# Performance work log

Measured on AMD Instinct MI355X. Metric: run time of the kernel, lower is better.

Reference implementation:

```python
import jax, jax.numpy as jnp
import numpy as np

EMBED = 128   # embed_dim
HEADS = 8
POINTS = 4
H_SP, W_SP = 51, 102   # hardcoded spatial_shapes in __init__
BEV = 100              # bev_res
HRES = 50              # height_res


def _make_ref_points():
    """Exact numpy replica of the spherical grid built in __init__."""
    eps = 1e-6
    x = np.linspace(-71 / 2, 71 / 2, BEV)
    y = np.linspace(-71 / 2, 71 / 2, BEV)
    z = np.linspace(-50 / 2, 50 / 2, HRES)
    gx, gy, gz = np.meshgrid(x, y, z, indexing='ij')
    phi = np.sign(gy + eps) * np.arccos(gx / (np.sqrt(gx ** 2 + gy ** 2) + eps))
    theta = np.arccos(gz / (np.sqrt(gx ** 2 + gy ** 2 + gz ** 2) + eps))
    phi = 2 * np.pi - phi
    phi[phi > 2 * np.pi] -= 2 * np.pi
    col = phi / (2 * np.pi)   # grd_col_cross
    row = theta / np.pi       # grd_row_cross
    ref = np.stack([col, row], axis=-1)              # (BEV, BEV, HRES, 2)
    ref = ref.transpose(2, 0, 1, 3).reshape(HRES, BEV * BEV, 2)
    return jnp.asarray(ref, dtype=jnp.float32)


def setup_inputs() -> dict:
    key = jax.random.key(0)
    ks = jax.random.split(key, 12)
    d = EMBED
    s = 0.02
    return {
        'query': jax.random.normal(ks[0], (1, BEV * BEV, d), jnp.float32),
        'value': jax.random.normal(ks[1], (1, H_SP * W_SP, d), jnp.float32),
        'ref_points': _make_ref_points(),
        'W_off': jax.random.normal(ks[2], (d, HEADS * POINTS * 2), jnp.float32) * s,
        'b_off': jax.random.normal(ks[3], (HEADS * POINTS * 2,), jnp.float32) * s,
        'W_attn': jax.random.normal(ks[4], (d, HEADS * POINTS), jnp.float32) * s,
        'b_attn': jax.random.normal(ks[5], (HEADS * POINTS,), jnp.float32) * s,
        'W_val': jax.random.normal(ks[6], (d, d), jnp.float32) * s,
        'b_val': jax.random.normal(ks[7], (d,), jnp.float32) * s,
        'W_out': jax.random.normal(ks[8], (d, d), jnp.float32) * s,
        'b_out': jax.random.normal(ks[9], (d,), jnp.float32) * s,
        'W_proj': jax.random.normal(ks[10], (d, 1), jnp.float32) * s,
        'b_proj': jax.random.normal(ks[11], (1,), jnp.float32) * s,
    }


def _bilinear_sample(vflat, loc):
    """grid_sample(bilinear, zero padding, align_corners=False).
    vflat: (B, H*W, hd) value maps; loc: (B, N, 2) normalized [0,1] (x,y)."""
    px = loc[..., 0] * W_SP - 0.5
    py = loc[..., 1] * H_SP - 0.5
    x0 = jnp.floor(px)
    y0 = jnp.floor(py)
    dx = (px - x0)[..., None]
    dy = (py - y0)[..., None]
    x0i = x0.astype(jnp.int32)
    y0i = y0.astype(jnp.int32)

    def gather(xi, yi):
        valid = (xi >= 0) & (xi < W_SP) & (yi >= 0) & (yi < H_SP)
        idx = jnp.clip(yi, 0, H_SP - 1) * W_SP + jnp.clip(xi, 0, W_SP - 1)
        v = jnp.take_along_axis(vflat, idx[..., None], axis=1)  # (B, N, hd)
        return v * valid[..., None].astype(vflat.dtype)

    v00 = gather(x0i, y0i)
    v01 = gather(x0i + 1, y0i)
    v10 = gather(x0i, y0i + 1)
    v11 = gather(x0i + 1, y0i + 1)
    return (v00 * (1 - dx) * (1 - dy) + v01 * dx * (1 - dy)
            + v10 * (1 - dx) * dy + v11 * dx * dy)


def reference(query, value, ref_points, W_off, b_off, W_attn, b_attn,
              W_val, b_val, W_out, b_out, W_proj, b_proj):
    bs, nq, d = query.shape
    hd = d // HEADS
    L = ref_points.shape[0]

    # query-dependent MSDA projections (identical across height levels)
    offsets = (query @ W_off + b_off).reshape(bs, nq, HEADS, POINTS, 2)
    aw = jax.nn.softmax((query @ W_attn + b_attn).reshape(bs, nq, HEADS, POINTS), axis=-1)
    awt = aw.transpose(0, 2, 1, 3)                              # (bs, heads, nq, points)
    v = (value @ W_val + b_val).reshape(bs, -1, HEADS, hd)
    vflat = v.transpose(0, 2, 1, 3).reshape(bs * HEADS, H_SP * W_SP, hd)
    norm = jnp.asarray([W_SP, H_SP], dtype=query.dtype)         # offset_normalizer [W, H]

    def per_level(ref):  # ref: (nq, 2) -> MSDA output with its internal residual
        loc = ref[None, :, None, None, :] + offsets / norm      # (bs, nq, heads, pts, 2)
        loc = loc.transpose(0, 2, 1, 3, 4).reshape(bs * HEADS, nq * POINTS, 2)
        samp = _bilinear_sample(vflat, loc).reshape(bs, HEADS, nq, POINTS, hd)
        out = jnp.einsum('bhnp,bhnpd->bnhd', awt, samp).reshape(bs, nq, d)
        return out @ W_out + b_out + query                      # mmcv MSDA adds identity

    grd = jax.vmap(per_level)(ref_points)                       # (L, bs, nq, d)
    grd_3d = grd.transpose(1, 2, 0, 3).reshape(bs, BEV, BEV, L, d)
    weights = jax.nn.softmax(grd_3d @ W_proj + b_proj, axis=3)  # (bs, BEV, BEV, L, 1)
    max_height_index = jnp.argmax(weights, axis=3)              # (bs, BEV, BEV, 1)
    grd_bev = (weights * grd_3d).sum(axis=3)                    # (bs, BEV, BEV, d)
    return grd_bev.reshape(bs, nq, d) + query, max_height_index
```

## Files before the change

### kernel.cpp

```cpp
#include <hip/hip_runtime.h>
#include <math.h>

#define EMBED   128
#define NHEADS  8
#define NPOINTS 4
#define HD      16
#define HSP     51
#define WSP     102
#define NPIX    (HSP * WSP)
#define NQ      10000
#define NLVL    50

#define GRID_A ((NPIX + 7) / 8)
#define GRID_B (NQ / 8)

__global__ __launch_bounds__(256) void k_prep(
    const float* __restrict__ value,
    const float* __restrict__ Wv,
    const float* __restrict__ bv,
    const float* __restrict__ query,
    const float* __restrict__ Woff,
    const float* __restrict__ boff,
    const float* __restrict__ Wattn,
    const float* __restrict__ battn,
    const float* __restrict__ Wout,
    const float* __restrict__ Wproj,
    float* __restrict__ vout,
    float* __restrict__ off_out,
    float* __restrict__ aw_out,
    float* __restrict__ u_out) {
    const int b = blockIdx.x;
    const int t = threadIdx.x;
    __shared__ float srow[8][EMBED];

    if (b < GRID_A) {
        const int p   = t >> 5;
        const int s   = t & 31;
        const int pix = b * 8 + p;
        const int pl  = min(pix, NPIX - 1);
        *(float4*)&srow[p][s * 4] =
            *(const float4*)(value + (size_t)pl * EMBED + s * 4);
        __syncthreads();
        float4 acc = *(const float4*)(bv + s * 4);
        const float* vr = srow[p];
        const float* wp = Wv + s * 4;
#pragma unroll 8
        for (int k = 0; k < EMBED; ++k) {
            const float qv = vr[k];
            const float4 w4 = *(const float4*)(wp + (size_t)k * EMBED);
            acc.x = fmaf(qv, w4.x, acc.x);
            acc.y = fmaf(qv, w4.y, acc.y);
            acc.z = fmaf(qv, w4.z, acc.z);
            acc.w = fmaf(qv, w4.w, acc.w);
        }
        if (pix < NPIX) {
            *(float4*)(vout + (size_t)pix * EMBED + s * 4) = acc;
        }
    } else if (b < GRID_A + GRID_B) {
        const int qi = t >> 5;
        const int s  = t & 31;
        const int q  = (b - GRID_A) * 8 + qi;
        *(float4*)&srow[qi][s * 4] =
            *(const float4*)(query + (size_t)q * EMBED + s * 4);
        __syncthreads();
        if (s < 24) {
            const float* vr = srow[qi];
            const float* wp;
            int wstride;
            float4 acc;
            if (s < 16) {
                wp = Woff + s * 4; wstride = 64;
                acc = *(const float4*)(boff + s * 4);
            } else {
                wp = Wattn + (s - 16) * 4; wstride = 32;
                acc = *(const float4*)(battn + (s - 16) * 4);
            }
#pragma unroll 8
            for (int k = 0; k < EMBED; ++k) {
                const float qv = vr[k];
                const float4 w4 = *(const float4*)(wp + (size_t)k * wstride);
                acc.x = fmaf(qv, w4.x, acc.x);
                acc.y = fmaf(qv, w4.y, acc.y);
                acc.z = fmaf(qv, w4.z, acc.z);
                acc.w = fmaf(qv, w4.w, acc.w);
            }
            if (s < 16) {
                *(float4*)(off_out + (size_t)q * 64 + s * 4) = acc;
            } else {
                const float mx = fmaxf(fmaxf(acc.x, acc.y), fmaxf(acc.z, acc.w));
                const float e0 = __expf(acc.x - mx), e1 = __expf(acc.y - mx);
                const float e2 = __expf(acc.z - mx), e3 = __expf(acc.w - mx);
                const float inv = 1.f / (e0 + e1 + e2 + e3);
                float4 r;
                r.x = e0 * inv; r.y = e1 * inv; r.z = e2 * inv; r.w = e3 * inv;
                *(float4*)(aw_out + (size_t)q * 32 + (s - 16) * 4) = r;
            }
        }
    } else {
        if (t < EMBED) {
            float acc = 0.f;
#pragma unroll 8
            for (int d = 0; d < EMBED; ++d)
                acc = fmaf(Wout[(size_t)t * EMBED + d], Wproj[d], acc);
            u_out[t] = acc;
        }
    }
}

__global__ __launch_bounds__(256, 4) void k_main(
    const float* __restrict__ query,
    const float* __restrict__ refp,
    const float* __restrict__ voff,
    const float* __restrict__ vaw,
    const float* __restrict__ vflat,
    const float* __restrict__ uvec,
    const float* __restrict__ Wout,
    const float* __restrict__ bout,
    float* __restrict__ out0,
    float* __restrict__ out1) {
    const int t = threadIdx.x;
    const int qslot = t >> 7;
    const int w2 = (t >> 6) & 1;
    const int half = (t >> 5) & 1;
    const int sub = t & 31;
    const int h  = sub >> 2;
    const int c4 = sub & 3;
    const int q = blockIdx.x * 2 + qslot;

    __shared__ float  s_rpy[2][NLVL];
    __shared__ float4 s_acc[2][32];
    __shared__ float  s_z[2], s_m[2];
    __shared__ int    s_b[2];

    if (t < 2 * NLVL) {
        const int ql = t / NLVL, l = t - ql * NLVL;
        const int qq = blockIdx.x * 2 + ql;
        s_rpy[ql][l] = refp[((size_t)l * NQ + qq) * 2 + 1];
    }

    const float4* offp = (const float4*)(voff + (size_t)q * 64 + h * 8);
    const float4 o01 = offp[0];
    const float4 o23 = offp[1];
    const float4 awv4 = *(const float4*)(vaw + (size_t)q * 32 + h * 4);
    const float4 u4 = *(const float4*)(uvec + h * 16 + c4 * 4);
    const float rpx = refp[(size_t)q * 2];
    const float4* vbase = (const float4*)vflat + h * 4 + c4;

    const float offx[4] = {o01.x, o01.z, o23.x, o23.z};
    const float offy[4] = {o01.y, o01.w, o23.y, o23.w};
    const float awv[4]  = {awv4.x, awv4.y, awv4.z, awv4.w};

    float wx0[NPOINTS], wx1[NPOINTS], oyc[NPOINTS];
    int xo0[NPOINTS], xo1[NPOINTS];
#pragma unroll
    for (int p = 0; p < NPOINTS; ++p) {
        const float px = fmaf(rpx, (float)WSP, offx[p]) - 0.5f;
        const float fx = floorf(px);
        const float dx = px - fx;
        const int x0 = (int)fx, x1 = x0 + 1;
        const float a = awv[p];
        wx0[p] = ((unsigned)x0 < (unsigned)WSP) ? a * (1.f - dx) : 0.f;
        wx1[p] = ((unsigned)x1 < (unsigned)WSP) ? a * dx : 0.f;
        xo0[p] = min(max(x0, 0), WSP - 1) * 32;
        xo1[p] = min(max(x1, 0), WSP - 1) * 32;
        oyc[p] = offy[p] - 0.5f;
    }

    __syncthreads();

    float4 acc = {0.f, 0.f, 0.f, 0.f};
    float Z = 0.f, m = -1e30f;
    int best = 0;

#pragma unroll 1
    for (int i = 0; i < 13; ++i) {
        if (4 * i + (w2 << 1) >= NLVL) break;
        const int l = 4 * i + (w2 << 1) + half;
        const float rpy = s_rpy[qslot][l];

        float4 v00[NPOINTS], v01[NPOINTS], v10[NPOINTS], v11[NPOINTS];
        float w00[NPOINTS], w01[NPOINTS], w10[NPOINTS], w11[NPOINTS];
#pragma unroll
        for (int p = 0; p < NPOINTS; ++p) {
            const float py = fmaf(rpy, (float)HSP, oyc[p]);
            const float fy = floorf(py);
            const float dy = py - fy;
            const int y0 = (int)fy, y1 = y0 + 1;
            const float t0 = ((unsigned)y0 < (unsigned)HSP) ? (1.f - dy) : 0.f;
            const float t1 = ((unsigned)y1 < (unsigned)HSP) ? dy : 0.f;
            const int rb0 = min(max(y0, 0), HSP - 1) * (WSP * 32);
            const int rb1 = min(max(y1, 0), HSP - 1) * (WSP * 32);
            v00[p] = vbase[rb0 + xo0[p]];
            v01[p] = vbase[rb0 + xo1[p]];
            v10[p] = vbase[rb1 + xo0[p]];
            v11[p] = vbase[rb1 + xo1[p]];
            w00[p] = wx0[p] * t0;
            w01[p] = wx1[p] * t0;
            w10[p] = wx0[p] * t1;
            w11[p] = wx1[p] * t1;
        }
        float4 s = {0.f, 0.f, 0.f, 0.f};
#pragma unroll
        for (int p = 0; p < NPOINTS; ++p) {
            s.x = fmaf(w00[p], v00[p].x, s.x); s.y = fmaf(w00[p], v00[p].y, s.y);
            s.z = fmaf(w00[p], v00[p].z, s.z); s.w = fmaf(w00[p], v00[p].w, s.w);
            s.x = fmaf(w01[p], v01[p].x, s.x); s.y = fmaf(w01[p], v01[p].y, s.y);
            s.z = fmaf(w01[p], v01[p].z, s.z); s.w = fmaf(w01[p], v01[p].w, s.w);
            s.x = fmaf(w10[p], v10[p].x, s.x); s.y = fmaf(w10[p], v10[p].y, s.y);
            s.z = fmaf(w10[p], v10[p].z, s.z); s.w = fmaf(w10[p], v10[p].w, s.w);
            s.x = fmaf(w11[p], v11[p].x, s.x); s.y = fmaf(w11[p], v11[p].y, s.y);
            s.z = fmaf(w11[p], v11[p].z, s.z); s.w = fmaf(w11[p], v11[p].w, s.w);
        }
        float part = s.x * u4.x;
        part = fmaf(s.y, u4.y, part);
        part = fmaf(s.z, u4.z, part);
        part = fmaf(s.w, u4.w, part);
#pragma unroll
        for (int d = 1; d < 32; d <<= 1)
            part += __shfl_xor(part, d, 64);
        const float e = __expf(part);
        Z += e;
        acc.x = fmaf(e, s.x, acc.x);
        acc.y = fmaf(e, s.y, acc.y);
        acc.z = fmaf(e, s.z, acc.z);
        acc.w = fmaf(e, s.w, acc.w);
        best = (part > m) ? l : best;
        m = fmaxf(part, m);
    }

    {
        const float mo = __shfl_xor(m, 32, 64);
        const int   bo = __shfl_xor(best, 32, 64);
        const float Zo = __shfl_xor(Z, 32, 64);
        const float ax = __shfl_xor(acc.x, 32, 64);
        const float ay = __shfl_xor(acc.y, 32, 64);
        const float az = __shfl_xor(acc.z, 32, 64);
        const float aw_ = __shfl_xor(acc.w, 32, 64);
        const bool takeOther = (mo > m) || (mo == m && bo < best);
        best = takeOther ? bo : best;
        m = fmaxf(m, mo);
        Z += Zo;
        acc.x += ax; acc.y += ay; acc.z += az; acc.w += aw_;
    }

    if (w2 == 1) {
        if (half == 0) s_acc[qslot][sub] = acc;
        if ((t & 63) == 0) { s_z[qslot] = Z; s_m[qslot] = m; s_b[qslot] = best; }
    }
    __syncthreads();

    if (w2 == 0) {
        const float4 ao = s_acc[qslot][sub];
        const float Zo = s_z[qslot];
        const float mo = s_m[qslot];
        const int   bo = s_b[qslot];
        const bool takeOther = (mo > m) || (mo == m && bo < best);
        best = takeOther ? bo : best;
        Z += Zo;
        acc.x += ao.x; acc.y += ao.y; acc.z += ao.z; acc.w += ao.w;

        const float inv = 1.f / Z;
        if (half == 0) {
            float4 sv;
            sv.x = acc.x * inv; sv.y = acc.y * inv;
            sv.z = acc.z * inv; sv.w = acc.w * inv;
            s_acc[qslot][sub] = sv;
            if (sub == 0) out1[q] = (float)best;
        }

        const int dpb = sub * 4;
        float4 r = {0.f, 0.f, 0.f, 0.f};
        if (half == 0) {
            const float4 b4 = *(const float4*)(bout + dpb);
            const float4 q4 = *(const float4*)(query + (size_t)q * EMBED + dpb);
            r.x = fmaf(2.f, q4.x, b4.x);
            r.y = fmaf(2.f, q4.y, b4.y);
            r.z = fmaf(2.f, q4.z, b4.z);
            r.w = fmaf(2.f, q4.w, b4.w);
        }
        const float4* srow = s_acc[qslot];
        const int cg0 = half * 16;
#pragma unroll 4
        for (int cg = cg0; cg < cg0 + 16; ++cg) {
            const float4 s4 = srow[cg];
            const float4 w0 = *(const float4*)(Wout + (size_t)(cg * 4 + 0) * EMBED + dpb);
            const float4 w1 = *(const float4*)(Wout + (size_t)(cg * 4 + 1) * EMBED + dpb);
            const float4 w2v = *(const float4*)(Wout + (size_t)(cg * 4 + 2) * EMBED + dpb);
            const float4 w3 = *(const float4*)(Wout + (size_t)(cg * 4 + 3) * EMBED + dpb);
            r.x = fmaf(s4.x, w0.x, r.x); r.y = fmaf(s4.x, w0.y, r.y);
            r.z = fmaf(s4.x, w0.z, r.z); r.w = fmaf(s4.x, w0.w, r.w);
            r.x = fmaf(s4.y, w1.x, r.x); r.y = fmaf(s4.y, w1.y, r.y);
            r.z = fmaf(s4.y, w1.z, r.z); r.w = fmaf(s4.y, w1.w, r.w);
            r.x = fmaf(s4.z, w2v.x, r.x); r.y = fmaf(s4.z, w2v.y, r.y);
            r.z = fmaf(s4.z, w2v.z, r.z); r.w = fmaf(s4.z, w2v.w, r.w);
            r.x = fmaf(s4.w, w3.x, r.x); r.y = fmaf(s4.w, w3.y, r.y);
            r.z = fmaf(s4.w, w3.z, r.z); r.w = fmaf(s4.w, w3.w, r.w);
        }
        {
            const float rx = __shfl_xor(r.x, 32, 64);
            const float ry = __shfl_xor(r.y, 32, 64);
            const float rz = __shfl_xor(r.z, 32, 64);
            const float rw = __shfl_xor(r.w, 32, 64);
            r.x += rx; r.y += ry; r.z += rz; r.w += rw;
        }
        if (half == 0)
            *(float4*)(out0 + (size_t)q * EMBED + dpb) = r;
    }
}

extern "C" void kernel_launch(void* const* d_in, const int* in_sizes, int n_in,
                              void* d_out, int out_size, void* d_ws, size_t ws_size,
                              hipStream_t stream) {
    const float* query = (const float*)d_in[0];
    const float* value = (const float*)d_in[1];
    const float* refp  = (const float*)d_in[2];
    const float* Woff  = (const float*)d_in[3];
    const float* boff  = (const float*)d_in[4];
    const float* Wattn = (const float*)d_in[5];
    const float* battn = (const float*)d_in[6];
    const float* Wval  = (const float*)d_in[7];
    const float* bval  = (const float*)d_in[8];
    const float* Wout  = (const float*)d_in[9];
    const float* bout  = (const float*)d_in[10];
    const float* Wproj = (const float*)d_in[11];

    float* ws = (float*)d_ws;
    float* ws_v   = ws;
    float* ws_off = ws_v + (size_t)NPIX * EMBED;
    float* ws_aw  = ws_off + (size_t)NQ * 64;
    float* ws_u   = ws_aw + (size_t)NQ * 32;

    float* out0 = (float*)d_out;
    float* out1 = out0 + (size_t)NQ * EMBED;

    hipLaunchKernelGGL(k_prep, dim3(GRID_A + GRID_B + 1), dim3(256), 0, stream,
                       value, Wval, bval, query, Woff, boff, Wattn, battn,
                       Wout, Wproj, ws_v, ws_off, ws_aw, ws_u);
    hipLaunchKernelGGL(k_main, dim3(NQ / 2), dim3(256), 0, stream,
                       query, refp, ws_off, ws_aw, ws_v, ws_u, Wout, bout,
                       out0, out1);
}
```

Measured before the change: 250.5 us.

## Precompute per-head projection score map to decouple softmax from value sampling

Precomputes, in the prep kernel, a per-pixel per-head scalar map g = v·u (value projected onto Wout·Wproj), so the height-softmax logits can be obtained by bilinearly sampling this scalar map instead of reducing the full sampled vectors. The main kernel now runs a cheap first pass computing the logits, max and argmax from the scalar map, stores the exp weights in shared memory, then runs the full vector sampling pass using those weights. This removes the dot-product and shuffle reduction from the heavy loop, and launch bounds are raised to allow more resident blocks. Every prep block now recomputes u redundantly, and the extra gather pass adds memory traffic.

```diff
diff --git a/kernel.cpp b/kernel.cpp
--- a/kernel.cpp
+++ b/kernel.cpp
@@ -26,12 +26,13 @@
     const float* __restrict__ Wout,
     const float* __restrict__ Wproj,
     float* __restrict__ vout,
+    float* __restrict__ gout,
     float* __restrict__ off_out,
-    float* __restrict__ aw_out,
-    float* __restrict__ u_out) {
+    float* __restrict__ aw_out) {
     const int b = blockIdx.x;
     const int t = threadIdx.x;
     __shared__ float srow[8][EMBED];
+    __shared__ float4 u_s[32];
 
     if (b < GRID_A) {
         const int p   = t >> 5;
@@ -40,6 +41,30 @@
         const int pl  = min(pix, NPIX - 1);
         *(float4*)&srow[p][s * 4] =
             *(const float4*)(value + (size_t)pl * EMBED + s * 4);
+        if (t < 32) {
+            float4 u4 = {0.f, 0.f, 0.f, 0.f};
+            const float* w0 = Wout + (size_t)(t * 4 + 0) * EMBED;
+            const float* w1 = Wout + (size_t)(t * 4 + 1) * EMBED;
+            const float* w2 = Wout + (size_t)(t * 4 + 2) * EMBED;
+            const float* w3 = Wout + (size_t)(t * 4 + 3) * EMBED;
+#pragma unroll 4
+            for (int d = 0; d < EMBED; d += 4) {
+                const float4 wp = *(const float4*)(Wproj + d);
+                const float4 a = *(const float4*)(w0 + d);
+                const float4 c = *(const float4*)(w1 + d);
+                const float4 e = *(const float4*)(w2 + d);
+                const float4 f = *(const float4*)(w3 + d);
+                u4.x = fmaf(a.x, wp.x, u4.x); u4.x = fmaf(a.y, wp.y, u4.x);
+                u4.x = fmaf(a.z, wp.z, u4.x); u4.x = fmaf(a.w, wp.w, u4.x);
+                u4.y = fmaf(c.x, wp.x, u4.y); u4.y = fmaf(c.y, wp.y, u4.y);
+                u4.y = fmaf(c.z, wp.z, u4.y); u4.y = fmaf(c.w, wp.w, u4.y);
+                u4.z = fmaf(e.x, wp.x, u4.z); u4.z = fmaf(e.y, wp.y, u4.z);
+                u4.z = fmaf(e.z, wp.z, u4.z); u4.z = fmaf(e.w, wp.w, u4.z);
+                u4.w = fmaf(f.x, wp.x, u4.w); u4.w = fmaf(f.y, wp.y, u4.w);
+                u4.w = fmaf(f.z, wp.z, u4.w); u4.w = fmaf(f.w, wp.w, u4.w);
+            }
+            u_s[t] = u4;
+        }
         __syncthreads();
         float4 acc = *(const float4*)(bv + s * 4);
         const float* vr = srow[p];
@@ -53,8 +78,17 @@
             acc.z = fmaf(qv, w4.z, acc.z);
             acc.w = fmaf(qv, w4.w, acc.w);
         }
+        const float4 u4 = u_s[s];
+        float gp = acc.x * u4.x;
+        gp = fmaf(acc.y, u4.y, gp);
+        gp = fmaf(acc.z, u4.z, gp);
+        gp = fmaf(acc.w, u4.w, gp);
+        gp += __shfl_xor(gp, 1, 64);
+        gp += __shfl_xor(gp, 2, 64);
         if (pix < NPIX) {
             *(float4*)(vout + (size_t)pix * EMBED + s * 4) = acc;
+            if ((s & 3) == 0)
+                gout[(size_t)pix * NHEADS + (s >> 2)] = gp;
         }
     } else if (b < GRID_A + GRID_B) {
         const int qi = t >> 5;
@@ -96,24 +130,16 @@
                 *(float4*)(aw_out + (size_t)q * 32 + (s - 16) * 4) = r;
             }
         }
-    } else {
-        if (t < EMBED) {
-            float acc = 0.f;
-#pragma unroll 8
-            for (int d = 0; d < EMBED; ++d)
-                acc = fmaf(Wout[(size_t)t * EMBED + d], Wproj[d], acc);
-            u_out[t] = acc;
-        }
     }
 }
 
-__global__ __launch_bounds__(256, 4) void k_main(
+__global__ __launch_bounds__(256, 6) void k_main(
     const float* __restrict__ query,
     const float* __restrict__ refp,
     const float* __restrict__ voff,
     const float* __restrict__ vaw,
     const float* __restrict__ vflat,
-    const float* __restrict__ uvec,
+    const float* __restrict__ gmap,
     const float* __restrict__ Wout,
     const float* __restrict__ bout,
     float* __restrict__ out0,
@@ -131,6 +157,7 @@
     __shared__ float4 s_acc[2][32];
     __shared__ float  s_z[2], s_m[2];
     __shared__ int    s_b[2];
+    __shared__ float  s_e[2][2][2][13];
 
     if (t < 2 * NLVL) {
         const int ql = t / NLVL, l = t - ql * NLVL;
@@ -142,7 +169,6 @@
     const float4 o01 = offp[0];
     const float4 o23 = offp[1];
     const float4 awv4 = *(const float4*)(vaw + (size_t)q * 32 + h * 4);
-    const float4 u4 = *(const float4*)(uvec + h * 16 + c4 * 4);
     const float rpx = refp[(size_t)q * 2];
     const float4* vbase = (const float4*)vflat + h * 4 + c4;
 
@@ -166,15 +192,59 @@
         oyc[p] = offy[p] - 0.5f;
     }
 
+    const float offx_c = (c4 == 0) ? o01.x : (c4 == 1) ? o01.z : (c4 == 2) ? o23.x : o23.z;
+    const float offy_c = (c4 == 0) ? o01.y : (c4 == 1) ? o01.w : (c4 == 2) ? o23.y : o23.w;
+    const float a_c    = (c4 == 0) ? awv4.x : (c4 == 1) ? awv4.y : (c4 == 2) ? awv4.z : awv4.w;
+    const float pxc = fmaf(rpx, (float)WSP, offx_c) - 0.5f;
+    const float fxc = floorf(pxc);
+    const float dxc = pxc - fxc;
+    const int x0c = (int)fxc, x1c = x0c + 1;
+    const float gwx0 = ((unsigned)x0c < (unsigned)WSP) ? a_c * (1.f - dxc) : 0.f;
+    const float gwx1 = ((unsigned)x1c < (unsigned)WSP) ? a_c * dxc : 0.f;
+    const int gx0 = min(max(x0c, 0), WSP - 1) * NHEADS + h;
+    const int gx1 = min(max(x1c, 0), WSP - 1) * NHEADS + h;
+    const float oyc_c = offy_c - 0.5f;
+
     __syncthreads();
 
-    float4 acc = {0.f, 0.f, 0.f, 0.f};
+    const int niter = 13 - w2;
     float Z = 0.f, m = -1e30f;
     int best = 0;
 
+#pragma unroll
+    for (int i = 0; i < 13; ++i) {
+        if (i >= niter) break;
+        const int l = 4 * i + (w2 << 1) + half;
+        const float rpy = s_rpy[qslot][l];
+        const float py = fmaf(rpy, (float)HSP, oyc_c);
+        const float fy = floorf(py);
+        const float dy = py - fy;
+        const int y0 = (int)fy, y1 = y0 + 1;
+        const float t0 = ((unsigned)y0 < (unsigned)HSP) ? (1.f - dy) : 0.f;
+        const float t1 = ((unsigned)y1 < (unsigned)HSP) ? dy : 0.f;
+        const int r0 = min(max(y0, 0), HSP - 1) * (WSP * NHEADS);
+        const int r1 = min(max(y1, 0), HSP - 1) * (WSP * NHEADS);
+        const float g00 = gmap[r0 + gx0];
+        const float g01 = gmap[r0 + gx1];
+        const float g10 = gmap[r1 + gx0];
+        const float g11 = gmap[r1 + gx1];
+        float row0 = gwx0 * g00; row0 = fmaf(gwx1, g01, row0);
+        float row1 = gwx0 * g10; row1 = fmaf(gwx1, g11, row1);
+        float pg = t0 * row0; pg = fmaf(t1, row1, pg);
+#pragma unroll
+        for (int d = 1; d < 32; d <<= 1)
+            pg += __shfl_xor(pg, d, 64);
+        const float e = __expf(pg);
+        Z += e;
+        best = (pg > m) ? l : best;
+        m = fmaxf(pg, m);
+        if (sub == 0) s_e[qslot][w2][half][i] = e;
+    }
+
+    float4 acc = {0.f, 0.f, 0.f, 0.f};
+
 #pragma unroll 1
-    for (int i = 0; i < 13; ++i) {
-        if (4 * i + (w2 << 1) >= NLVL) break;
+    for (int i = 0; i < niter; ++i) {
         const int l = 4 * i + (w2 << 1) + half;
         const float rpy = s_rpy[qslot][l];
 
@@ -211,21 +281,11 @@
             s.x = fmaf(w11[p], v11[p].x, s.x); s.y = fmaf(w11[p], v11[p].y, s.y);
             s.z = fmaf(w11[p], v11[p].z, s.z); s.w = fmaf(w11[p], v11[p].w, s.w);
         }
-        float part = s.x * u4.x;
-        part = fmaf(s.y, u4.y, part);
-        part = fmaf(s.z, u4.z, part);
-        part = fmaf(s.w, u4.w, part);
-#pragma unroll
-        for (int d = 1; d < 32; d <<= 1)
-            part += __shfl_xor(part, d, 64);
-        const float e = __expf(part);
-        Z += e;
+        const float e = s_e[qslot][w2][half][i];
         acc.x = fmaf(e, s.x, acc.x);
         acc.y = fmaf(e, s.y, acc.y);
         acc.z = fmaf(e, s.z, acc.z);
         acc.w = fmaf(e, s.w, acc.w);
-        best = (part > m) ? l : best;
-        m = fmaxf(part, m);
     }
 
     {
@@ -326,17 +386,17 @@
 
     float* ws = (float*)d_ws;
     float* ws_v   = ws;
-    float* ws_off = ws_v + (size_t)NPIX * EMBED;
+    float* ws_g   = ws_v + (size_t)NPIX * EMBED;
+    float* ws_off = ws_g + (size_t)NPIX * NHEADS;
     float* ws_aw  = ws_off + (size_t)NQ * 64;
-    float* ws_u   = ws_aw + (size_t)NQ * 32;
 
     float* out0 = (float*)d_out;
     float* out1 = out0 + (size_t)NQ * EMBED;
 
-    hipLaunchKernelGGL(k_prep, dim3(GRID_A + GRID_B + 1), dim3(256), 0, stream,
+    hipLaunchKernelGGL(k_prep, dim3(GRID_A + GRID_B), dim3(256), 0, stream,
                        value, Wval, bval, query, Woff, boff, Wattn, battn,
-                       Wout, Wproj, ws_v, ws_off, ws_aw, ws_u);
+                       Wout, Wproj, ws_v, ws_g, ws_off, ws_aw);
     hipLaunchKernelGGL(k_main, dim3(NQ / 2), dim3(256), 0, stream,
-                       query, refp, ws_off, ws_aw, ws_v, ws_u, Wout, bout,
+                       query, refp, ws_off, ws_aw, ws_v, ws_g, Wout, bout,
                        out0, out1);
 }
```

New measurement: 292.7 us. +16.8%, slower.

## Pad projected value map with zero border to drop bilinear bounds checks

Applied to the files above, without the earlier changes.

The value projection now writes into a zero-padded grid (54x105 slots, one-pixel border of zeros), so the sampling loop clamps coordinates with fmed3 and indexes directly, with no per-corner validity tests or index clamps. This removes integer compare/select and min/max work from the hot gather loop. k_main launch bounds are also raised to request 8 blocks per CU, which may constrain registers and cause spills. Clamping to [-1, W] relies on the padded border to reproduce zero-padding semantics at the edges.

```diff
diff --git a/kernel.cpp b/kernel.cpp
--- a/kernel.cpp
+++ b/kernel.cpp
@@ -11,7 +11,12 @@
 #define NQ      10000
 #define NLVL    50
 
-#define GRID_A ((NPIX + 7) / 8)
+#define PROW 54
+#define PCOL 105
+#define NSLOT (PROW * PCOL)
+#define ROWQ  (PCOL * 32)
+
+#define GRID_A ((NSLOT + 7) / 8)
 #define GRID_B (NQ / 8)
 
 __global__ __launch_bounds__(256) void k_prep(
@@ -34,28 +39,36 @@
     __shared__ float srow[8][EMBED];
 
     if (b < GRID_A) {
-        const int p   = t >> 5;
-        const int s   = t & 31;
-        const int pix = b * 8 + p;
-        const int pl  = min(pix, NPIX - 1);
-        *(float4*)&srow[p][s * 4] =
-            *(const float4*)(value + (size_t)pl * EMBED + s * 4);
+        const int p    = t >> 5;
+        const int s    = t & 31;
+        const int slot = b * 8 + p;
+        const int prow = slot / PCOL;
+        const int pcol = slot - prow * PCOL;
+        const bool inb   = slot < NSLOT;
+        const bool valid = inb && prow >= 1 && prow <= HSP
+                               && pcol >= 1 && pcol <= WSP;
+        const int pix = (prow - 1) * WSP + (pcol - 1);
+        if (valid)
+            *(float4*)&srow[p][s * 4] =
+                *(const float4*)(value + (size_t)pix * EMBED + s * 4);
         __syncthreads();
-        float4 acc = *(const float4*)(bv + s * 4);
-        const float* vr = srow[p];
-        const float* wp = Wv + s * 4;
+        float4 acc = {0.f, 0.f, 0.f, 0.f};
+        if (valid) {
+            acc = *(const float4*)(bv + s * 4);
+            const float* vr = srow[p];
+            const float* wp = Wv + s * 4;
 #pragma unroll 8
-        for (int k = 0; k < EMBED; ++k) {
-            const float qv = vr[k];
-            const float4 w4 = *(const float4*)(wp + (size_t)k * EMBED);
-            acc.x = fmaf(qv, w4.x, acc.x);
-            acc.y = fmaf(qv, w4.y, acc.y);
-            acc.z = fmaf(qv, w4.z, acc.z);
-            acc.w = fmaf(qv, w4.w, acc.w);
-        }
-        if (pix < NPIX) {
-            *(float4*)(vout + (size_t)pix * EMBED + s * 4) = acc;
-        }
+            for (int k = 0; k < EMBED; ++k) {
+                const float qv = vr[k];
+                const float4 w4 = *(const float4*)(wp + (size_t)k * EMBED);
+                acc.x = fmaf(qv, w4.x, acc.x);
+                acc.y = fmaf(qv, w4.y, acc.y);
+                acc.z = fmaf(qv, w4.z, acc.z);
+                acc.w = fmaf(qv, w4.w, acc.w);
+            }
+        }
+        if (inb)
+            *(float4*)(vout + (size_t)slot * EMBED + s * 4) = acc;
     } else if (b < GRID_A + GRID_B) {
         const int qi = t >> 5;
         const int s  = t & 31;
@@ -107,7 +120,7 @@
     }
 }
 
-__global__ __launch_bounds__(256, 4) void k_main(
+__global__ __launch_bounds__(256, 8) void k_main(
     const float* __restrict__ query,
     const float* __restrict__ refp,
     const float* __restrict__ voff,
@@ -144,7 +157,7 @@
     const float4 awv4 = *(const float4*)(vaw + (size_t)q * 32 + h * 4);
     const float4 u4 = *(const float4*)(uvec + h * 16 + c4 * 4);
     const float rpx = refp[(size_t)q * 2];
-    const float4* vbase = (const float4*)vflat + h * 4 + c4;
+    const float4* vbase = (const float4*)vflat + sub;
 
     const float offx[4] = {o01.x, o01.z, o23.x, o23.z};
     const float offy[4] = {o01.y, o01.w, o23.y, o23.w};
@@ -155,14 +168,15 @@
 #pragma unroll
     for (int p = 0; p < NPOINTS; ++p) {
         const float px = fmaf(rpx, (float)WSP, offx[p]) - 0.5f;
-        const float fx = floorf(px);
-        const float dx = px - fx;
-        const int x0 = (int)fx, x1 = x0 + 1;
+        const float pxc = __builtin_amdgcn_fmed3f(px, -1.f, (float)WSP);
+        const float fx = floorf(pxc);
+        const float dx = pxc - fx;
+        const int x0 = (int)fx;
         const float a = awv[p];
-        wx0[p] = ((unsigned)x0 < (unsigned)WSP) ? a * (1.f - dx) : 0.f;
-        wx1[p] = ((unsigned)x1 < (unsigned)WSP) ? a * dx : 0.f;
-        xo0[p] = min(max(x0, 0), WSP - 1) * 32;
-        xo1[p] = min(max(x1, 0), WSP - 1) * 32;
+        wx0[p] = a * (1.f - dx);
+        wx1[p] = a * dx;
+        xo0[p] = (x0 + 1) * 32;
+        xo1[p] = xo0[p] + 32;
         oyc[p] = offy[p] - 0.5f;
     }
 
@@ -183,21 +197,21 @@
 #pragma unroll
         for (int p = 0; p < NPOINTS; ++p) {
             const float py = fmaf(rpy, (float)HSP, oyc[p]);
-            const float fy = floorf(py);
-            const float dy = py - fy;
-            const int y0 = (int)fy, y1 = y0 + 1;
-            const float t0 = ((unsigned)y0 < (unsigned)HSP) ? (1.f - dy) : 0.f;
-            const float t1 = ((unsigned)y1 < (unsigned)HSP) ? dy : 0.f;
-            const int rb0 = min(max(y0, 0), HSP - 1) * (WSP * 32);
-            const int rb1 = min(max(y1, 0), HSP - 1) * (WSP * 32);
+            const float pyc = __builtin_amdgcn_fmed3f(py, -1.f, (float)HSP);
+            const float fy = floorf(pyc);
+            const float dy = pyc - fy;
+            const int y0 = (int)fy;
+            const int rb0 = (y0 + 1) * ROWQ;
+            const int rb1 = rb0 + ROWQ;
+            const float t0 = 1.f - dy;
             v00[p] = vbase[rb0 + xo0[p]];
             v01[p] = vbase[rb0 + xo1[p]];
             v10[p] = vbase[rb1 + xo0[p]];
             v11[p] = vbase[rb1 + xo1[p]];
             w00[p] = wx0[p] * t0;
             w01[p] = wx1[p] * t0;
-            w10[p] = wx0[p] * t1;
-            w11[p] = wx1[p] * t1;
+            w10[p] = wx0[p] * dy;
+            w11[p] = wx1[p] * dy;
         }
         float4 s = {0.f, 0.f, 0.f, 0.f};
 #pragma unroll
@@ -326,7 +340,7 @@
 
     float* ws = (float*)d_ws;
     float* ws_v   = ws;
-    float* ws_off = ws_v + (size_t)NPIX * EMBED;
+    float* ws_off = ws_v + (size_t)NSLOT * EMBED;
     float* ws_aw  = ws_off + (size_t)NQ * 64;
     float* ws_u   = ws_aw + (size_t)NQ * 32;
 
```

Measured after the change: 263.4 us. +5.1%, slower.
